# Kernel tuning notes

Hardware: AMD Instinct MI355X
Metric: run time of the kernel (lower is better)

The kernel has to match this reference:

```python
import jax, jax.numpy as jnp
import numpy as np

N = 8192
F_IN = 128
F_OUT = 128
NEG_SLOPE = 0.2


def setup_inputs() -> dict:
    key = jax.random.key(0)
    k_h, k_adj, k_W, k_a = jax.random.split(key, 4)
    h = jax.random.normal(k_h, (N, F_IN), dtype=jnp.float32)
    # binary adjacency mask as float (the module multiplies scores by adj)
    adj = (jax.random.uniform(k_adj, (N, N)) < 0.05).astype(jnp.float32)
    # nn.Linear(in, out, bias=False): weight shape [out, in]
    W = jax.random.normal(k_W, (F_OUT, F_IN), dtype=jnp.float32) / np.sqrt(F_IN)
    # nn.Linear(2*out, 1, bias=False): weight shape [1, 2*out]
    a = jax.random.normal(k_a, (1, 2 * F_OUT), dtype=jnp.float32) / np.sqrt(2 * F_OUT)
    return {"h": h, "adj": adj, "W": W, "a": a}


def reference(h, adj, W, a):
    # Wh: [N, F_out]
    Wh = h @ W.T
    f = Wh.shape[-1]
    # a([Wh_i ; Wh_j]) factored: e[i, j] = leaky_relu(Wh[i]@a1 + Wh[j]@a2)
    a1 = a[0, :f]  # [F_out]
    a2 = a[0, f:]  # [F_out]
    s_i = Wh @ a1  # [N]
    s_j = Wh @ a2  # [N]
    e = jax.nn.leaky_relu(s_i[:, None] + s_j[None, :], NEG_SLOPE)  # [N, N]
    # faithful to original: softmax over dim=1 of e * adj (multiplicative mask)
    attention = jax.nn.softmax(e * adj, axis=1)  # [N, N]
    return attention @ Wh  # [N, F_out]
```

## Files before the change

kernel.cpp:

```cpp
#include <hip/hip_runtime.h>

#define N_NODES 8192
#define FDIM 128
#define NEG_SLOPE 0.2f
#define SEG 512

__global__ __launch_bounds__(256) void wh_fused_kernel(
    const float* __restrict__ h, const float* __restrict__ W,
    float* __restrict__ Wh, float* __restrict__ S) {
  __shared__ float Wt[FDIM * 132];
  __shared__ float rows[32 * 132];
  const int t = threadIdx.x;
  const int base = blockIdx.x * 32;
  for (int it = 0; it < 64; ++it) {
    int idx = t + 256 * it;
    int o = idx >> 7, k = idx & 127;
    Wt[k * 132 + o] = W[idx];
  }
  for (int it = 0; it < 16; ++it) {
    int idx = t + 256 * it;
    int r = idx >> 7, col = idx & 127;
    rows[r * 132 + col] = h[(size_t)base * FDIM + idx];
  }
  __syncthreads();
  const int c4 = (t & 31) * 4;
  const int g = t >> 5;
  float acc[4][4];
#pragma unroll
  for (int rr = 0; rr < 4; ++rr)
#pragma unroll
    for (int cc = 0; cc < 4; ++cc) acc[rr][cc] = 0.f;
  for (int k = 0; k < FDIM; ++k) {
    float4 wv = *(const float4*)&Wt[k * 132 + c4];
    float rv[4];
#pragma unroll
    for (int rr = 0; rr < 4; ++rr) rv[rr] = rows[(4 * g + rr) * 132 + k];
#pragma unroll
    for (int rr = 0; rr < 4; ++rr) {
      acc[rr][0] += rv[rr] * wv.x;
      acc[rr][1] += rv[rr] * wv.y;
      acc[rr][2] += rv[rr] * wv.z;
      acc[rr][3] += rv[rr] * wv.w;
    }
  }
#pragma unroll
  for (int rr = 0; rr < 4; ++rr) {
    int r = base + 4 * g + rr;
    *(float4*)&Wh[(size_t)r * FDIM + c4] =
        make_float4(acc[rr][0], acc[rr][1], acc[rr][2], acc[rr][3]);
  }
  __syncthreads();
  float4 cs = make_float4(acc[0][0] + acc[1][0] + acc[2][0] + acc[3][0],
                          acc[0][1] + acc[1][1] + acc[2][1] + acc[3][1],
                          acc[0][2] + acc[1][2] + acc[2][2] + acc[3][2],
                          acc[0][3] + acc[1][3] + acc[2][3] + acc[3][3]);
  *(float4*)&rows[g * FDIM + c4] = cs;
  __syncthreads();
  if (t < FDIM) {
    float s = 0.f;
#pragma unroll
    for (int gg = 0; gg < 8; ++gg) s += rows[gg * FDIM + t];
    atomicAdd(&S[t], s);
  }
}

__global__ __launch_bounds__(256) void scores_kernel(
    const float* __restrict__ Wh, const float* __restrict__ a,
    float* __restrict__ s1, float* __restrict__ s2) {
  const int t = threadIdx.x;
  const int lane = t & 63;
  const int wave = t >> 6;
  const int row = blockIdx.x * 4 + wave;
  float v0 = Wh[(size_t)row * FDIM + lane];
  float v1 = Wh[(size_t)row * FDIM + 64 + lane];
  float d1 = v0 * a[lane] + v1 * a[64 + lane];
  float d2 = v0 * a[FDIM + lane] + v1 * a[FDIM + 64 + lane];
  for (int off = 32; off; off >>= 1) {
    d1 += __shfl_down(d1, off);
    d2 += __shfl_down(d2, off);
  }
  if (lane == 0) { s1[row] = d1; s2[row] = d2; }
}

__global__ __launch_bounds__(256) void gat_row_kernel(
    const float* __restrict__ adj, const float* __restrict__ Wh,
    const float* __restrict__ s1, const float* __restrict__ s2,
    const float* __restrict__ S, float* __restrict__ out) {
  const int i = blockIdx.x;
  const int t = threadIdx.x;
  const int lane = t & 63;
  const int wave = t >> 6;
  __shared__ float2 pairs[4 * SEG];
  __shared__ int counts[4];
  __shared__ float red[4];
  __shared__ float red2[4];
  __shared__ float fpart[4][FDIM];

  const float s1i = s1[i];
  const float4* __restrict__ arow = (const float4*)(adj + (size_t)i * N_NODES);
  float2* __restrict__ mypairs = pairs + wave * SEG;
  const unsigned long long lmask = (1ull << lane) - 1ull;

  float4 av[8];
#pragma unroll
  for (int it = 0; it < 8; ++it) av[it] = arow[it * 256 + t];
  int cbase = 0;
#pragma unroll
  for (int it = 0; it < 8; ++it) {
    const int j4 = it * 256 + t;
    float v[4] = {av[it].x, av[it].y, av[it].z, av[it].w};
#pragma unroll
    for (int c = 0; c < 4; ++c) {
      bool pred = (v[c] != 0.f);
      unsigned long long b = __ballot(pred);
      if (pred) {
        int pos = cbase + (int)__popcll(b & lmask);
        if (pos < SEG) ((int*)&mypairs[pos])[1] = j4 * 4 + c;
      }
      cbase += (int)__popcll(b);
    }
  }
  const int mycnt = cbase < SEG ? cbase : SEG;
  if (lane == 0) counts[wave] = mycnt;

  float lmax = -1e30f;
  for (int k = lane; k < mycnt; k += 64) {
    int j = ((const int*)&mypairs[k])[1];
    float e = s1i + s2[j];
    e = e > 0.f ? e : NEG_SLOPE * e;
    mypairs[k].x = e;
    lmax = fmaxf(lmax, e);
  }
  for (int off = 32; off; off >>= 1) lmax = fmaxf(lmax, __shfl_down(lmax, off));
  if (lane == 0) red[wave] = lmax;
  __syncthreads();
  const int cnt = counts[0] + counts[1] + counts[2] + counts[3];
  float m = fmaxf(fmaxf(red[0], red[1]), fmaxf(red[2], red[3]));
  if (cnt < N_NODES) m = fmaxf(m, 0.f);
  const float em = __expf(-m);

  float lsum = 0.f;
  for (int k = lane; k < mycnt; k += 64) {
    float p = __expf(mypairs[k].x - m);
    mypairs[k].x = p;
    lsum += p;
  }
  for (int off = 32; off; off >>= 1) lsum += __shfl_down(lsum, off);
  if (lane == 0) red2[wave] = lsum;

  const int half = lane >> 5, lq = lane & 31;
  const float4* __restrict__ Wh4 = (const float4*)Wh;
  float ax = 0.f, ay = 0.f, az = 0.f, aw = 0.f;
  const int nit = (mycnt + 1) >> 1;
  int it = 0;
  for (; it + 3 < nit; it += 4) {
#pragma unroll
    for (int c = 0; c < 4; ++c) {
      int p = 2 * (it + c) + half;
      bool ok = p < mycnt;
      float2 pr = mypairs[ok ? p : 0];
      int j = ((const int*)&pr)[1];
      float4 v = Wh4[((size_t)j << 5) + lq];
      float w = ok ? pr.x - em : 0.f;
      ax += w * v.x; ay += w * v.y; az += w * v.z; aw += w * v.w;
    }
  }
  for (; it < nit; ++it) {
    int p = 2 * it + half;
    bool ok = p < mycnt;
    float2 pr = mypairs[ok ? p : 0];
    int j = ((const int*)&pr)[1];
    float4 v = Wh4[((size_t)j << 5) + lq];
    float w = ok ? pr.x - em : 0.f;
    ax += w * v.x; ay += w * v.y; az += w * v.z; aw += w * v.w;
  }
  ax += __shfl_down(ax, 32);
  ay += __shfl_down(ay, 32);
  az += __shfl_down(az, 32);
  aw += __shfl_down(aw, 32);
  if (lane < 32)
    *(float4*)&fpart[wave][4 * lq] = make_float4(ax, ay, az, aw);
  __syncthreads();
  if (t < FDIM) {
    float l = red2[0] + red2[1] + red2[2] + red2[3]
              + (float)(N_NODES - cnt) * em;
    float o = (fpart[0][t] + fpart[1][t] + fpart[2][t] + fpart[3][t]
               + em * S[t]) / l;
    out[(size_t)i * FDIM + t] = o;
  }
}

extern "C" void kernel_launch(void* const* d_in, const int* in_sizes, int n_in,
                              void* d_out, int out_size, void* d_ws, size_t ws_size,
                              hipStream_t stream) {
  const float* h   = (const float*)d_in[0];
  const float* adj = (const float*)d_in[1];
  const float* W   = (const float*)d_in[2];
  const float* a   = (const float*)d_in[3];
  float* out = (float*)d_out;
  float* Wh = (float*)d_ws;
  float* s1 = Wh + (size_t)N_NODES * FDIM;
  float* s2 = s1 + N_NODES;
  float* S  = s2 + N_NODES;

  hipMemsetAsync(S, 0, FDIM * sizeof(float), stream);
  hipLaunchKernelGGL(wh_fused_kernel, dim3(N_NODES / 32), dim3(256), 0, stream,
                     h, W, Wh, S);
  hipLaunchKernelGGL(scores_kernel, dim3(N_NODES / 4), dim3(256), 0, stream,
                     Wh, a, s1, s2);
  hipLaunchKernelGGL(gat_row_kernel, dim3(N_NODES), dim3(256), 0, stream,
                     adj, Wh, s1, s2, S, out);
}
```

Measured before the change: 444.8 us.

## Fuse score computation into Wh GEMM and use a global max bound for single-pass softmax

Computes s1/s2 inside the Wh projection kernel by reducing the accumulator tile against a, and records a global max of s2 via an order-preserving atomicMax key. This removes the separate scores kernel. The row kernel then takes the softmax shift as leaky_relu(s1_i + max s2), clamped at zero, instead of reducing a per-row max. That lets it compute exponentials during the adjacency scan and drain the Wh gather incrementally, interleaved with prefetching the next adj/s2 chunk. It drops a block barrier and the extra passes over shared memory, but it evaluates exp for every column rather than only nonzeros. The looser shift is still an upper bound on the row maximum, so it is numerically safe.

```diff
diff --git a/kernel.cpp b/kernel.cpp
--- a/kernel.cpp
+++ b/kernel.cpp
@@ -5,9 +5,16 @@
 #define NEG_SLOPE 0.2f
 #define SEG 512
 
+__device__ inline unsigned fkey(float x) {
+  unsigned b = __float_as_uint(x);
+  return (b & 0x80000000u) ? ~b : (b | 0x80000000u);
+}
+
 __global__ __launch_bounds__(256) void wh_fused_kernel(
     const float* __restrict__ h, const float* __restrict__ W,
-    float* __restrict__ Wh, float* __restrict__ S) {
+    const float* __restrict__ a, float* __restrict__ Wh,
+    float* __restrict__ s1g, float* __restrict__ s2g,
+    float* __restrict__ S, unsigned* __restrict__ s2max_key) {
   __shared__ float Wt[FDIM * 132];
   __shared__ float rows[32 * 132];
   const int t = threadIdx.x;
@@ -49,6 +56,36 @@
     *(float4*)&Wh[(size_t)r * FDIM + c4] =
         make_float4(acc[rr][0], acc[rr][1], acc[rr][2], acc[rr][3]);
   }
+  {
+    float4 a1c = *(const float4*)&a[c4];
+    float4 a2c = *(const float4*)&a[FDIM + c4];
+    float p1[4], p2[4];
+#pragma unroll
+    for (int rr = 0; rr < 4; ++rr) {
+      p1[rr] = acc[rr][0] * a1c.x + acc[rr][1] * a1c.y +
+               acc[rr][2] * a1c.z + acc[rr][3] * a1c.w;
+      p2[rr] = acc[rr][0] * a2c.x + acc[rr][1] * a2c.y +
+               acc[rr][2] * a2c.z + acc[rr][3] * a2c.w;
+    }
+#pragma unroll
+    for (int rr = 0; rr < 4; ++rr)
+      for (int off = 16; off; off >>= 1) {
+        p1[rr] += __shfl_down(p1[rr], off, 32);
+        p2[rr] += __shfl_down(p2[rr], off, 32);
+      }
+    if ((t & 31) == 0) {
+      unsigned kmax = 0;
+#pragma unroll
+      for (int rr = 0; rr < 4; ++rr) {
+        int r = base + 4 * g + rr;
+        s1g[r] = p1[rr];
+        s2g[r] = p2[rr];
+        unsigned kk = fkey(p2[rr]);
+        kmax = kk > kmax ? kk : kmax;
+      }
+      atomicMax(s2max_key, kmax);
+    }
+  }
   __syncthreads();
   float4 cs = make_float4(acc[0][0] + acc[1][0] + acc[2][0] + acc[3][0],
                           acc[0][1] + acc[1][1] + acc[2][1] + acc[3][1],
@@ -64,124 +101,109 @@
   }
 }
 
-__global__ __launch_bounds__(256) void scores_kernel(
-    const float* __restrict__ Wh, const float* __restrict__ a,
-    float* __restrict__ s1, float* __restrict__ s2) {
-  const int t = threadIdx.x;
-  const int lane = t & 63;
-  const int wave = t >> 6;
-  const int row = blockIdx.x * 4 + wave;
-  float v0 = Wh[(size_t)row * FDIM + lane];
-  float v1 = Wh[(size_t)row * FDIM + 64 + lane];
-  float d1 = v0 * a[lane] + v1 * a[64 + lane];
-  float d2 = v0 * a[FDIM + lane] + v1 * a[FDIM + 64 + lane];
-  for (int off = 32; off; off >>= 1) {
-    d1 += __shfl_down(d1, off);
-    d2 += __shfl_down(d2, off);
-  }
-  if (lane == 0) { s1[row] = d1; s2[row] = d2; }
-}
-
 __global__ __launch_bounds__(256) void gat_row_kernel(
     const float* __restrict__ adj, const float* __restrict__ Wh,
     const float* __restrict__ s1, const float* __restrict__ s2,
-    const float* __restrict__ S, float* __restrict__ out) {
+    const unsigned* __restrict__ s2max_key, const float* __restrict__ S,
+    float* __restrict__ out) {
   const int i = blockIdx.x;
   const int t = threadIdx.x;
   const int lane = t & 63;
   const int wave = t >> 6;
   __shared__ float2 pairs[4 * SEG];
   __shared__ int counts[4];
-  __shared__ float red[4];
   __shared__ float red2[4];
   __shared__ float fpart[4][FDIM];
 
   const float s1i = s1[i];
+  unsigned kk = *s2max_key;
+  unsigned bb = (kk & 0x80000000u) ? (kk ^ 0x80000000u) : ~kk;
+  float pm = s1i + __uint_as_float(bb);
+  pm = pm > 0.f ? pm : NEG_SLOPE * pm;
+  const float m = fmaxf(pm, 0.f);
+  const float em = __expf(-m);
+
   const float4* __restrict__ arow = (const float4*)(adj + (size_t)i * N_NODES);
+  const float4* __restrict__ s2v = (const float4*)s2;
   float2* __restrict__ mypairs = pairs + wave * SEG;
   const unsigned long long lmask = (1ull << lane) - 1ull;
-
-  float4 av[8];
-#pragma unroll
-  for (int it = 0; it < 8; ++it) av[it] = arow[it * 256 + t];
-  int cbase = 0;
+  const int half = lane >> 5, lq = lane & 31;
+  const float4* __restrict__ Wh4 = (const float4*)Wh;
+
+  int cbase = 0, drained = 0;
+  float lsum = 0.f;
+  float ax = 0.f, ay = 0.f, az = 0.f, aw = 0.f;
+
+  float4 av = arow[t], sv = s2v[t];
 #pragma unroll
   for (int it = 0; it < 8; ++it) {
+    float4 avn, svn;
+    if (it < 7) {
+      avn = arow[(it + 1) * 256 + t];
+      svn = s2v[(it + 1) * 256 + t];
+    }
     const int j4 = it * 256 + t;
-    float v[4] = {av[it].x, av[it].y, av[it].z, av[it].w};
+    float vv[4] = {av.x, av.y, av.z, av.w};
+    float ss[4] = {sv.x, sv.y, sv.z, sv.w};
 #pragma unroll
     for (int c = 0; c < 4; ++c) {
-      bool pred = (v[c] != 0.f);
+      bool pred = (vv[c] != 0.f);
+      float e = s1i + ss[c];
+      e = e > 0.f ? e : NEG_SLOPE * e;
+      float p = __expf(e - m);
       unsigned long long b = __ballot(pred);
       if (pred) {
         int pos = cbase + (int)__popcll(b & lmask);
-        if (pos < SEG) ((int*)&mypairs[pos])[1] = j4 * 4 + c;
+        if (pos < SEG)
+          mypairs[pos] = make_float2(p - em, __int_as_float(j4 * 4 + c));
       }
+      lsum += pred ? p : 0.f;
       cbase += (int)__popcll(b);
     }
-  }
-  const int mycnt = cbase < SEG ? cbase : SEG;
-  if (lane == 0) counts[wave] = mycnt;
-
-  float lmax = -1e30f;
-  for (int k = lane; k < mycnt; k += 64) {
-    int j = ((const int*)&mypairs[k])[1];
-    float e = s1i + s2[j];
-    e = e > 0.f ? e : NEG_SLOPE * e;
-    mypairs[k].x = e;
-    lmax = fmaxf(lmax, e);
-  }
-  for (int off = 32; off; off >>= 1) lmax = fmaxf(lmax, __shfl_down(lmax, off));
-  if (lane == 0) red[wave] = lmax;
-  __syncthreads();
-  const int cnt = counts[0] + counts[1] + counts[2] + counts[3];
-  float m = fmaxf(fmaxf(red[0], red[1]), fmaxf(red[2], red[3]));
-  if (cnt < N_NODES) m = fmaxf(m, 0.f);
-  const float em = __expf(-m);
-
-  float lsum = 0.f;
-  for (int k = lane; k < mycnt; k += 64) {
-    float p = __expf(mypairs[k].x - m);
-    mypairs[k].x = p;
-    lsum += p;
-  }
-  for (int off = 32; off; off >>= 1) lsum += __shfl_down(lsum, off);
-  if (lane == 0) red2[wave] = lsum;
-
-  const int half = lane >> 5, lq = lane & 31;
-  const float4* __restrict__ Wh4 = (const float4*)Wh;
-  float ax = 0.f, ay = 0.f, az = 0.f, aw = 0.f;
-  const int nit = (mycnt + 1) >> 1;
-  int it = 0;
-  for (; it + 3 < nit; it += 4) {
-#pragma unroll
-    for (int c = 0; c < 4; ++c) {
-      int p = 2 * (it + c) + half;
-      bool ok = p < mycnt;
-      float2 pr = mypairs[ok ? p : 0];
-      int j = ((const int*)&pr)[1];
-      float4 v = Wh4[((size_t)j << 5) + lq];
-      float w = ok ? pr.x - em : 0.f;
+    av = avn; sv = svn;
+    int cc = cbase < SEG ? cbase : SEG;
+    while (drained + 8 <= cc) {
+      float2 pr0 = mypairs[drained + half];
+      float2 pr1 = mypairs[drained + 2 + half];
+      float2 pr2 = mypairs[drained + 4 + half];
+      float2 pr3 = mypairs[drained + 6 + half];
+      float4 v0 = Wh4[((size_t)__float_as_int(pr0.y) << 5) + lq];
+      float4 v1 = Wh4[((size_t)__float_as_int(pr1.y) << 5) + lq];
+      float4 v2 = Wh4[((size_t)__float_as_int(pr2.y) << 5) + lq];
+      float4 v3 = Wh4[((size_t)__float_as_int(pr3.y) << 5) + lq];
+      ax += pr0.x * v0.x + pr1.x * v1.x + pr2.x * v2.x + pr3.x * v3.x;
+      ay += pr0.x * v0.y + pr1.x * v1.y + pr2.x * v2.y + pr3.x * v3.y;
+      az += pr0.x * v0.z + pr1.x * v1.z + pr2.x * v2.z + pr3.x * v3.z;
+      aw += pr0.x * v0.w + pr1.x * v1.w + pr2.x * v2.w + pr3.x * v3.w;
+      drained += 8;
+    }
+  }
+  {
+    int cc = cbase < SEG ? cbase : SEG;
+    while (drained < cc) {
+      int p0 = drained + half;
+      bool ok = p0 < cc;
+      float2 pr = mypairs[ok ? p0 : 0];
+      float4 v = Wh4[((size_t)__float_as_int(pr.y) << 5) + lq];
+      float w = ok ? pr.x : 0.f;
       ax += w * v.x; ay += w * v.y; az += w * v.z; aw += w * v.w;
-    }
-  }
-  for (; it < nit; ++it) {
-    int p = 2 * it + half;
-    bool ok = p < mycnt;
-    float2 pr = mypairs[ok ? p : 0];
-    int j = ((const int*)&pr)[1];
-    float4 v = Wh4[((size_t)j << 5) + lq];
-    float w = ok ? pr.x - em : 0.f;
-    ax += w * v.x; ay += w * v.y; az += w * v.z; aw += w * v.w;
+      drained += 2;
+    }
   }
   ax += __shfl_down(ax, 32);
   ay += __shfl_down(ay, 32);
   az += __shfl_down(az, 32);
   aw += __shfl_down(aw, 32);
+  for (int off = 32; off; off >>= 1) lsum += __shfl_down(lsum, off);
+  if (lane == 0) {
+    red2[wave] = lsum;
+    counts[wave] = cbase < SEG ? cbase : SEG;
+  }
   if (lane < 32)
     *(float4*)&fpart[wave][4 * lq] = make_float4(ax, ay, az, aw);
   __syncthreads();
   if (t < FDIM) {
+    int cnt = counts[0] + counts[1] + counts[2] + counts[3];
     float l = red2[0] + red2[1] + red2[2] + red2[3]
               + (float)(N_NODES - cnt) * em;
     float o = (fpart[0][t] + fpart[1][t] + fpart[2][t] + fpart[3][t]
@@ -202,12 +224,11 @@
   float* s1 = Wh + (size_t)N_NODES * FDIM;
   float* s2 = s1 + N_NODES;
   float* S  = s2 + N_NODES;
-
-  hipMemsetAsync(S, 0, FDIM * sizeof(float), stream);
+  unsigned* s2max_key = (unsigned*)(S + FDIM);
+
+  hipMemsetAsync(S, 0, FDIM * sizeof(float) + sizeof(unsigned), stream);
   hipLaunchKernelGGL(wh_fused_kernel, dim3(N_NODES / 32), dim3(256), 0, stream,
-                     h, W, Wh, S);
-  hipLaunchKernelGGL(scores_kernel, dim3(N_NODES / 4), dim3(256), 0, stream,
-                     Wh, a, s1, s2);
+                     h, W, a, Wh, s1, s2, S, s2max_key);
   hipLaunchKernelGGL(gat_row_kernel, dim3(N_NODES), dim3(256), 0, stream,
-                     adj, Wh, s1, s2, S, out);
-}
+                     adj, Wh, s1, s2, s2max_key, S, out);
+}
```

New measurement: 464.2 us. +4.4%, slower.
